# Kernel tuning notes

Hardware: AMD Instinct MI355X
Metric: run time of the kernel (lower is better)

Reference implementation:

```python
import jax, jax.numpy as jnp
import numpy as np

NUM_HEADS = 16


def _qdq(x):
    """Symmetric int8 fake-quant along the last axis (per-token for
    activations, per-output-channel for [out,in] weights). Equivalent math to
    int8 GEMM with dynamic scales: (x_q @ w_q.T) * sx * sw == qdq(x) @ qdq(w).T."""
    s = jnp.maximum(jnp.max(jnp.abs(x), axis=-1, keepdims=True) / 127.0, 1e-8)
    return jnp.clip(jnp.round(x / s), -127.0, 127.0) * s


def setup_inputs() -> dict:
    key = jax.random.key(0)
    ks = jax.random.split(key, 8)
    B, N, M, D = 2, 4096, 512, 2048
    w_std = 0.02
    return {
        "x": jax.random.normal(ks[0], (B, N, D), jnp.float32),
        "cond": jax.random.normal(ks[1], (B, M, D), jnp.float32),
        "wq": jax.random.normal(ks[2], (D, D), jnp.float32) * w_std,
        "bq": jax.random.normal(ks[3], (D,), jnp.float32) * w_std,
        "wkv": jax.random.normal(ks[4], (2 * D, D), jnp.float32) * w_std,
        "bkv": jax.random.normal(ks[5], (2 * D,), jnp.float32) * w_std,
        "wp": jax.random.normal(ks[6], (D, D), jnp.float32) * w_std,
        "bp": jax.random.normal(ks[7], (D,), jnp.float32) * w_std,
    }


def reference(x, cond, wq, bq, wkv, bkv, wp, bp):
    B, N, C = x.shape
    M = cond.shape[1]
    H = NUM_HEADS
    Dh = C // H

    # W8A8 dynamic-scale q projection (per-token act quant, per-channel weight quant)
    q = _qdq(x) @ _qdq(wq).T + bq                      # [B,N,C]
    # fp16-style kv projection
    kv = cond @ wkv.T + bkv                            # [B,M,2C]
    k, v = jnp.split(kv, 2, axis=-1)                   # view(...,2,H,Dh).unbind(2)

    q = q.reshape(B, N, H, Dh)
    k = k.reshape(B, M, H, Dh)
    v = v.reshape(B, M, H, Dh)

    scale = 1.0 / np.sqrt(Dh)
    attn = jax.nn.softmax(jnp.einsum('bnhd,bmhd->bhnm', q, k) * scale, axis=-1)
    o = jnp.einsum('bhnm,bmhd->bnhd', attn, v).reshape(B, N, C)

    # fused quant_sum (per-token requant of attention output) + W8A8 proj
    out = _qdq(o) @ _qdq(wp).T + bp                    # [B,N,C]
    return out
```

## Files before the change

### kernel.cpp

```cpp
#include <hip/hip_runtime.h>
#include <cstdint>
#include <cstddef>


typedef __bf16 bf16_t;
typedef __bf16 bf16x8 __attribute__((ext_vector_type(8)));
typedef float f32x4 __attribute__((ext_vector_type(4)));

__device__ __forceinline__ void gld16(void* lds, const void* g) {
    __builtin_amdgcn_global_load_lds(
        (__attribute__((address_space(1))) uint32_t*)(uintptr_t)g,
        (__attribute__((address_space(3))) uint32_t*)(uint32_t)(uintptr_t)lds,
        16, 0, 0);
}

__device__ __forceinline__ void load8(const float* p, int i, float* v) {
    const float4* p4 = (const float4*)p;
    float4 a = p4[2 * i], b = p4[2 * i + 1];
    v[0] = a.x; v[1] = a.y; v[2] = a.z; v[3] = a.w;
    v[4] = b.x; v[5] = b.y; v[6] = b.z; v[7] = b.w;
}
__device__ __forceinline__ void load8(const bf16_t* p, int i, float* v) {
    bf16x8 t = ((const bf16x8*)p)[i];
#pragma unroll
    for (int j = 0; j < 8; ++j) v[j] = (float)t[j];
}

template <int QUANT, typename T>
__global__ __launch_bounds__(256) void rowpack(const T* __restrict__ in,
                                               bf16_t* __restrict__ out, int K) {
    const int tid = threadIdx.x;
    const size_t row = blockIdx.x;
    const T* rp = in + row * (size_t)K;
    const int n8 = K >> 3;
    float scale = 1.0f;
    if (QUANT) {
        float m = 0.f;
        for (int i = tid; i < n8; i += 256) {
            float v[8];
            load8(rp, i, v);
#pragma unroll
            for (int j = 0; j < 8; ++j) m = fmaxf(m, fabsf(v[j]));
        }
        __shared__ float red[256];
        red[tid] = m;
        __syncthreads();
        for (int s = 128; s > 0; s >>= 1) {
            if (tid < s) red[tid] = fmaxf(red[tid], red[tid + s]);
            __syncthreads();
        }
        scale = fmaxf(red[0] * (1.0f / 127.0f), 1e-8f);
    }
    const int KT = K >> 5;
    const int p = (int)(row >> 7), c = ((int)row >> 4) & 7, lm = (int)row & 15;
    for (int i = tid; i < n8; i += 256) {
        const int col = i << 3;
        const int kt = col >> 5, quad = (col >> 3) & 3;
        float v[8];
        load8(rp, i, v);
        bf16x8 o8;
#pragma unroll
        for (int j = 0; j < 8; ++j) {
            float q = v[j];
            if (QUANT) {
                q = rintf(q / scale);
                q = fminf(127.f, fmaxf(-127.f, q)) * scale;
            }
            o8[j] = (bf16_t)q;
        }
        const size_t dst = ((size_t)(p * KT + kt) * 8 + c) * 512 + (quad * 16 + lm) * 8;
        *(bf16x8*)(out + dst) = o8;
    }
}

template <int MODE>
__global__ __launch_bounds__(256) void gemm_pk(const bf16_t* __restrict__ A,
                                               const bf16_t* __restrict__ B,
                                               const float* __restrict__ bias,
                                               void* __restrict__ C,
                                               int N, int K) {
    __shared__ __align__(16) bf16_t sA[4096];
    __shared__ __align__(16) bf16_t sB[4096];

    const int tid = threadIdx.x;
    const int l = tid & 63, w = tid >> 6;
    const int lm = l & 15, quad = l >> 4;
    const int wm = w & 1, wn = w >> 1;
    const int KT = K >> 5;
    const size_t aBase = (size_t)blockIdx.y * KT * 8 * 512;
    const size_t bBase = (size_t)blockIdx.x * KT * 8 * 512;

    f32x4 acc[4][4] = {};
    for (int kt = 0; kt < KT; ++kt) {
        __syncthreads();
#pragma unroll
        for (int it = 0; it < 2; ++it) {
            const int c = w + it * 4;
            gld16(sA + c * 512, A + aBase + ((size_t)kt * 8 + c) * 512 + l * 8);
            gld16(sB + c * 512, B + bBase + ((size_t)kt * 8 + c) * 512 + l * 8);
        }
        __syncthreads();
        bf16x8 af[4], bfr[4];
#pragma unroll
        for (int i = 0; i < 4; ++i)
            af[i] = *(const bf16x8*)(sA + (wm * 4 + i) * 512 + l * 8);
#pragma unroll
        for (int j = 0; j < 4; ++j)
            bfr[j] = *(const bf16x8*)(sB + (wn * 4 + j) * 512 + l * 8);
#pragma unroll
        for (int i = 0; i < 4; ++i)
#pragma unroll
            for (int j = 0; j < 4; ++j)
                acc[i][j] = __builtin_amdgcn_mfma_f32_16x16x32_bf16(af[i], bfr[j], acc[i][j], 0, 0, 0);
    }
#pragma unroll
    for (int i = 0; i < 4; ++i) {
#pragma unroll
        for (int j = 0; j < 4; ++j) {
            const int col = blockIdx.x * 128 + wn * 64 + j * 16 + lm;
            const float bv = bias[col];
#pragma unroll
            for (int r = 0; r < 4; ++r) {
                const int row = blockIdx.y * 128 + wm * 64 + i * 16 + quad * 4 + r;
                const float v = acc[i][j][r] + bv;
                if (MODE == 1) {
                    ((float*)C)[(size_t)row * N + col] = v;
                } else if (MODE == 0) {
                    const int b = row >> 12, n = row & 4095;
                    const int h = col >> 7, d = col & 127;
                    const int p = n >> 6, mt = (n >> 4) & 3, lmq = n & 15;
                    const int kq = d >> 5, qq = (d >> 3) & 3, jq = d & 7;
                    const size_t idx =
                        (((size_t)(b * 16 + h) * 64 + p) * 16 + kq * 4 + mt) * 512 +
                        (qq * 16 + lmq) * 8 + jq;
                    ((bf16_t*)C)[idx] = (bf16_t)v;
                } else {
                    const int b = row >> 9, m = row & 511;
                    const int half = col >> 11, h = (col >> 7) & 15, d = col & 127;
                    const int t8 = m >> 6;
                    bf16_t* out = (bf16_t*)C;
                    if (half == 0) {
                        const int nt = (m >> 4) & 3, lmk = m & 15;
                        const int kc = d >> 5, qk = (d >> 3) & 3, jk = d & 7;
                        const size_t idx =
                            (((size_t)(b * 16 + h) * 8 + t8) * 16 + kc * 4 + nt) * 512 +
                            (qk * 16 + lmk) * 8 + jk;
                        out[idx] = (bf16_t)v;
                    } else {
                        const int kv2 = (m >> 5) & 1, qv = (m >> 3) & 3, jv = m & 7;
                        const int ntv = d >> 4, lmv = d & 15;
                        const size_t idx = 2097152 +
                            (((size_t)(b * 16 + h) * 8 + t8) * 16 + kv2 * 8 + ntv) * 512 +
                            (qv * 16 + lmv) * 8 + jv;
                        out[idx] = (bf16_t)v;
                    }
                }
            }
        }
    }
}

__global__ __launch_bounds__(256, 2) void attn64(const bf16_t* __restrict__ qpk,
                                                 const bf16_t* __restrict__ kvpk,
                                                 bf16_t* __restrict__ o) {
    constexpr float SCALE = 0.08838834764831845f;
    __shared__ __align__(16) bf16_t sQ[8192];
    __shared__ __align__(16) bf16_t sKV[8192];
    __shared__ __align__(16) bf16_t sP[4096];
    __shared__ float redM[4][64];
    __shared__ float redS[4][64];

    const int tid = threadIdx.x;
    const int l = tid & 63, w = tid >> 6;
    const int lm = l & 15, quad = l >> 4;
    const int b = blockIdx.z, h = blockIdx.y;
    const int p = blockIdx.x;
    const int bh = b * 16 + h;
    const size_t qbase = ((size_t)bh * 64 + p) * 8192;
    const size_t kbase = (size_t)bh * 65536;
    const size_t vbase = 2097152 + (size_t)bh * 65536;

#pragma unroll
    for (int it = 0; it < 4; ++it) {
        const int c = it * 4 + w;
        gld16(sQ + c * 512, qpk + qbase + (size_t)c * 512 + l * 8);
    }

    f32x4 sfr[8][4] = {};
#pragma unroll
    for (int t8 = 0; t8 < 8; ++t8) {
        __syncthreads();
#pragma unroll
        for (int it = 0; it < 4; ++it) {
            const int c = it * 4 + w;
            gld16(sKV + c * 512, kvpk + kbase + ((size_t)t8 * 16 + c) * 512 + l * 8);
        }
        __syncthreads();
#pragma unroll
        for (int kc = 0; kc < 4; ++kc) {
            bf16x8 bb = *(const bf16x8*)(sKV + (kc * 4 + w) * 512 + l * 8);
#pragma unroll
            for (int mt = 0; mt < 4; ++mt) {
                bf16x8 aa = *(const bf16x8*)(sQ + (kc * 4 + mt) * 512 + l * 8);
                sfr[t8][mt] = __builtin_amdgcn_mfma_f32_16x16x32_bf16(aa, bb, sfr[t8][mt], 0, 0, 0);
            }
        }
    }

    float inv[4][4];
    {
        float mymax[4][4];
#pragma unroll
        for (int mt = 0; mt < 4; ++mt)
#pragma unroll
            for (int r = 0; r < 4; ++r) {
                float m = -3.0e38f;
#pragma unroll
                for (int t8 = 0; t8 < 8; ++t8) m = fmaxf(m, sfr[t8][mt][r]);
                m = fmaxf(m, __shfl_xor(m, 1));
                m = fmaxf(m, __shfl_xor(m, 2));
                m = fmaxf(m, __shfl_xor(m, 4));
                m = fmaxf(m, __shfl_xor(m, 8));
                mymax[mt][r] = m;
            }
        if (lm == 0) {
#pragma unroll
            for (int mt = 0; mt < 4; ++mt)
#pragma unroll
                for (int r = 0; r < 4; ++r)
                    redM[w][mt * 16 + quad * 4 + r] = mymax[mt][r];
        }
        __syncthreads();
#pragma unroll
        for (int mt = 0; mt < 4; ++mt)
#pragma unroll
            for (int r = 0; r < 4; ++r) {
                const int row = mt * 16 + quad * 4 + r;
                const float M =
                    fmaxf(fmaxf(redM[0][row], redM[1][row]), fmaxf(redM[2][row], redM[3][row])) *
                    SCALE;
                float s = 0.f;
#pragma unroll
                for (int t8 = 0; t8 < 8; ++t8) {
                    const float pe = __expf(sfr[t8][mt][r] * SCALE - M);
                    sfr[t8][mt][r] = pe;
                    s += pe;
                }
                s += __shfl_xor(s, 1);
                s += __shfl_xor(s, 2);
                s += __shfl_xor(s, 4);
                s += __shfl_xor(s, 8);
                if (lm == 0) redS[w][row] = s;
            }
        __syncthreads();
#pragma unroll
        for (int mt = 0; mt < 4; ++mt)
#pragma unroll
            for (int r = 0; r < 4; ++r) {
                const int row = mt * 16 + quad * 4 + r;
                inv[mt][r] = 1.f / (redS[0][row] + redS[1][row] + redS[2][row] + redS[3][row]);
            }
    }

    f32x4 oc[4][2] = {};
    const int ktd = w >> 1;
    const int quadd = (w & 1) * 2 + (lm >> 3);
    const int jd = lm & 7;
#pragma unroll
    for (int t8 = 0; t8 < 8; ++t8) {
        __syncthreads();
#pragma unroll
        for (int mt = 0; mt < 4; ++mt)
#pragma unroll
            for (int r = 0; r < 4; ++r)
                sP[(mt * 2 + ktd) * 512 + (quadd * 16 + quad * 4 + r) * 8 + jd] =
                    (bf16_t)sfr[t8][mt][r];
#pragma unroll
        for (int it = 0; it < 4; ++it) {
            const int c = it * 4 + w;
            gld16(sKV + c * 512, kvpk + vbase + ((size_t)t8 * 16 + c) * 512 + l * 8);
        }
        __syncthreads();
#pragma unroll
        for (int kv = 0; kv < 2; ++kv) {
            bf16x8 aa[4];
#pragma unroll
            for (int mt = 0; mt < 4; ++mt)
                aa[mt] = *(const bf16x8*)(sP + (mt * 2 + kv) * 512 + l * 8);
#pragma unroll
            for (int ni = 0; ni < 2; ++ni) {
                bf16x8 bb = *(const bf16x8*)(sKV + (kv * 8 + w * 2 + ni) * 512 + l * 8);
#pragma unroll
                for (int mt = 0; mt < 4; ++mt)
                    oc[mt][ni] = __builtin_amdgcn_mfma_f32_16x16x32_bf16(aa[mt], bb, oc[mt][ni], 0, 0, 0);
            }
        }
    }

#pragma unroll
    for (int mt = 0; mt < 4; ++mt)
#pragma unroll
        for (int ni = 0; ni < 2; ++ni)
#pragma unroll
            for (int r = 0; r < 4; ++r) {
                const int row = mt * 16 + quad * 4 + r;
                const int d = w * 32 + ni * 16 + lm;
                o[((size_t)b * 4096 + p * 64 + row) * 2048 + h * 128 + d] =
                    (bf16_t)(oc[mt][ni][r] * inv[mt][r]);
            }
}

extern "C" void kernel_launch(void* const* d_in, const int* in_sizes, int n_in,
                              void* d_out, int out_size, void* d_ws, size_t ws_size,
                              hipStream_t stream) {
    (void)in_sizes; (void)n_in; (void)out_size; (void)ws_size;
    const float* x    = (const float*)d_in[0];
    const float* cond = (const float*)d_in[1];
    const float* wq   = (const float*)d_in[2];
    const float* bq   = (const float*)d_in[3];
    const float* wkv  = (const float*)d_in[4];
    const float* bkv  = (const float*)d_in[5];
    const float* wp   = (const float*)d_in[6];
    const float* bp   = (const float*)d_in[7];

    const size_t MB = 1ull << 20;
    uint8_t* ws = (uint8_t*)d_ws;
    bf16_t* qxpk   = (bf16_t*)(ws + 0);
    bf16_t* qpk    = (bf16_t*)(ws + 32 * MB);
    bf16_t* wqpk   = (bf16_t*)(ws + 64 * MB);
    bf16_t* wkvpk  = (bf16_t*)(ws + 72 * MB);
    bf16_t* wppk   = (bf16_t*)(ws + 88 * MB);
    bf16_t* condpk = (bf16_t*)(ws + 96 * MB);
    bf16_t* kvpk   = (bf16_t*)(ws + 100 * MB);
    bf16_t* o_nat  = qxpk;
    bf16_t* opk    = qpk;

    dim3 blk(256);
    rowpack<1, float><<<8192, blk, 0, stream>>>(x, qxpk, 2048);
    rowpack<1, float><<<2048, blk, 0, stream>>>(wq, wqpk, 2048);
    rowpack<1, float><<<2048, blk, 0, stream>>>(wp, wppk, 2048);
    rowpack<0, float><<<1024, blk, 0, stream>>>(cond, condpk, 2048);
    rowpack<0, float><<<4096, blk, 0, stream>>>(wkv, wkvpk, 2048);
    gemm_pk<0><<<dim3(16, 64), blk, 0, stream>>>(qxpk, wqpk, bq, qpk, 2048, 2048);
    gemm_pk<2><<<dim3(32, 8), blk, 0, stream>>>(condpk, wkvpk, bkv, kvpk, 4096, 2048);
    attn64<<<dim3(64, 16, 2), blk, 0, stream>>>(qpk, kvpk, o_nat);
    rowpack<1, bf16_t><<<8192, blk, 0, stream>>>(o_nat, opk, 2048);
    gemm_pk<1><<<dim3(16, 64), blk, 0, stream>>>(opk, wppk, bp, (float*)d_out, 2048, 2048);
}
```

Baseline: 599.4 us.

## Double K-step per barrier in GEMMs and attention, split KV GEMM rows

The GEMM main loop now loads a 64-wide K slice (two 32-wide sub-steps) between barrier pairs, which halves the number of synchronisations. A new gemm_kv kernel uses 64-row tiles so the KV projection launches 512 blocks instead of 256, filling more CUs. The attention kernel loads 128 K/V rows per barrier and reuses the Q buffer for P, which doubles the KV staging buffer and keeps total LDS about the same. In exchange, each block uses more shared memory in the GEMMs, and gemm_kv keeps the A tile only half as large.

```diff
diff --git a/kernel.cpp b/kernel.cpp
--- a/kernel.cpp
+++ b/kernel.cpp
@@ -74,13 +74,47 @@
 }
 
 template <int MODE>
+__device__ __forceinline__ void epi_store(void* C, int N, int row, int col, float v) {
+    if (MODE == 1) {
+        ((float*)C)[(size_t)row * N + col] = v;
+    } else if (MODE == 0) {
+        const int b = row >> 12, n = row & 4095;
+        const int h = col >> 7, d = col & 127;
+        const int p = n >> 6, mt = (n >> 4) & 3, lmq = n & 15;
+        const int kq = d >> 5, qq = (d >> 3) & 3, jq = d & 7;
+        const size_t idx = (((size_t)(b * 16 + h) * 64 + p) * 16 + kq * 4 + mt) * 512 +
+                           (qq * 16 + lmq) * 8 + jq;
+        ((bf16_t*)C)[idx] = (bf16_t)v;
+    } else {
+        const int b = row >> 9, m = row & 511;
+        const int half = col >> 11, h = (col >> 7) & 15, d = col & 127;
+        const int t8 = m >> 6;
+        bf16_t* out = (bf16_t*)C;
+        if (half == 0) {
+            const int nt = (m >> 4) & 3, lmk = m & 15;
+            const int kc = d >> 5, qk = (d >> 3) & 3, jk = d & 7;
+            const size_t idx = (((size_t)(b * 16 + h) * 8 + t8) * 16 + kc * 4 + nt) * 512 +
+                               (qk * 16 + lmk) * 8 + jk;
+            out[idx] = (bf16_t)v;
+        } else {
+            const int kv2 = (m >> 5) & 1, qv = (m >> 3) & 3, jv = m & 7;
+            const int ntv = d >> 4, lmv = d & 15;
+            const size_t idx = 2097152 +
+                (((size_t)(b * 16 + h) * 8 + t8) * 16 + kv2 * 8 + ntv) * 512 +
+                (qv * 16 + lmv) * 8 + jv;
+            out[idx] = (bf16_t)v;
+        }
+    }
+}
+
+template <int MODE>
 __global__ __launch_bounds__(256) void gemm_pk(const bf16_t* __restrict__ A,
                                                const bf16_t* __restrict__ B,
                                                const float* __restrict__ bias,
                                                void* __restrict__ C,
                                                int N, int K) {
-    __shared__ __align__(16) bf16_t sA[4096];
-    __shared__ __align__(16) bf16_t sB[4096];
+    __shared__ __align__(16) bf16_t sA[8192];
+    __shared__ __align__(16) bf16_t sB[8192];
 
     const int tid = threadIdx.x;
     const int l = tid & 63, w = tid >> 6;
@@ -91,27 +125,32 @@
     const size_t bBase = (size_t)blockIdx.x * KT * 8 * 512;
 
     f32x4 acc[4][4] = {};
-    for (int kt = 0; kt < KT; ++kt) {
-        __syncthreads();
-#pragma unroll
-        for (int it = 0; it < 2; ++it) {
-            const int c = w + it * 4;
-            gld16(sA + c * 512, A + aBase + ((size_t)kt * 8 + c) * 512 + l * 8);
-            gld16(sB + c * 512, B + bBase + ((size_t)kt * 8 + c) * 512 + l * 8);
-        }
-        __syncthreads();
-        bf16x8 af[4], bfr[4];
-#pragma unroll
-        for (int i = 0; i < 4; ++i)
-            af[i] = *(const bf16x8*)(sA + (wm * 4 + i) * 512 + l * 8);
-#pragma unroll
-        for (int j = 0; j < 4; ++j)
-            bfr[j] = *(const bf16x8*)(sB + (wn * 4 + j) * 512 + l * 8);
-#pragma unroll
-        for (int i = 0; i < 4; ++i)
+    const int NIT = K >> 6;
+    for (int kt = 0; kt < NIT; ++kt) {
+        __syncthreads();
+#pragma unroll
+        for (int it = 0; it < 4; ++it) {
+            const int c = it * 4 + w;
+            gld16(sA + c * 512, A + aBase + ((size_t)kt * 16 + c) * 512 + l * 8);
+            gld16(sB + c * 512, B + bBase + ((size_t)kt * 16 + c) * 512 + l * 8);
+        }
+        __syncthreads();
+#pragma unroll
+        for (int h = 0; h < 2; ++h) {
+            bf16x8 af[4], bfr[4];
+#pragma unroll
+            for (int i = 0; i < 4; ++i)
+                af[i] = *(const bf16x8*)(sA + (h * 8 + wm * 4 + i) * 512 + l * 8);
 #pragma unroll
             for (int j = 0; j < 4; ++j)
-                acc[i][j] = __builtin_amdgcn_mfma_f32_16x16x32_bf16(af[i], bfr[j], acc[i][j], 0, 0, 0);
+                bfr[j] = *(const bf16x8*)(sB + (h * 8 + wn * 4 + j) * 512 + l * 8);
+#pragma unroll
+            for (int i = 0; i < 4; ++i)
+#pragma unroll
+                for (int j = 0; j < 4; ++j)
+                    acc[i][j] =
+                        __builtin_amdgcn_mfma_f32_16x16x32_bf16(af[i], bfr[j], acc[i][j], 0, 0, 0);
+        }
     }
 #pragma unroll
     for (int i = 0; i < 4; ++i) {
@@ -122,39 +161,73 @@
 #pragma unroll
             for (int r = 0; r < 4; ++r) {
                 const int row = blockIdx.y * 128 + wm * 64 + i * 16 + quad * 4 + r;
-                const float v = acc[i][j][r] + bv;
-                if (MODE == 1) {
-                    ((float*)C)[(size_t)row * N + col] = v;
-                } else if (MODE == 0) {
-                    const int b = row >> 12, n = row & 4095;
-                    const int h = col >> 7, d = col & 127;
-                    const int p = n >> 6, mt = (n >> 4) & 3, lmq = n & 15;
-                    const int kq = d >> 5, qq = (d >> 3) & 3, jq = d & 7;
-                    const size_t idx =
-                        (((size_t)(b * 16 + h) * 64 + p) * 16 + kq * 4 + mt) * 512 +
-                        (qq * 16 + lmq) * 8 + jq;
-                    ((bf16_t*)C)[idx] = (bf16_t)v;
-                } else {
-                    const int b = row >> 9, m = row & 511;
-                    const int half = col >> 11, h = (col >> 7) & 15, d = col & 127;
-                    const int t8 = m >> 6;
-                    bf16_t* out = (bf16_t*)C;
-                    if (half == 0) {
-                        const int nt = (m >> 4) & 3, lmk = m & 15;
-                        const int kc = d >> 5, qk = (d >> 3) & 3, jk = d & 7;
-                        const size_t idx =
-                            (((size_t)(b * 16 + h) * 8 + t8) * 16 + kc * 4 + nt) * 512 +
-                            (qk * 16 + lmk) * 8 + jk;
-                        out[idx] = (bf16_t)v;
-                    } else {
-                        const int kv2 = (m >> 5) & 1, qv = (m >> 3) & 3, jv = m & 7;
-                        const int ntv = d >> 4, lmv = d & 15;
-                        const size_t idx = 2097152 +
-                            (((size_t)(b * 16 + h) * 8 + t8) * 16 + kv2 * 8 + ntv) * 512 +
-                            (qv * 16 + lmv) * 8 + jv;
-                        out[idx] = (bf16_t)v;
-                    }
-                }
+                epi_store<MODE>(C, N, row, col, acc[i][j][r] + bv);
+            }
+        }
+    }
+}
+
+__global__ __launch_bounds__(256) void gemm_kv(const bf16_t* __restrict__ A,
+                                               const bf16_t* __restrict__ B,
+                                               const float* __restrict__ bias,
+                                               bf16_t* __restrict__ C,
+                                               int N, int K) {
+    __shared__ __align__(16) bf16_t sA[4096];
+    __shared__ __align__(16) bf16_t sB[8192];
+
+    const int tid = threadIdx.x;
+    const int l = tid & 63, w = tid >> 6;
+    const int lm = l & 15, quad = l >> 4;
+    const int wm = w & 1, wn = w >> 1;
+    const int KT = K >> 5;
+    const int p = blockIdx.y >> 1, hh = blockIdx.y & 1;
+    const size_t aPan = (size_t)p * KT * 8 * 512;
+    const size_t bBase = (size_t)blockIdx.x * KT * 8 * 512;
+
+    f32x4 acc[2][4] = {};
+    const int NIT = K >> 6;
+    for (int kt = 0; kt < NIT; ++kt) {
+        __syncthreads();
+#pragma unroll
+        for (int it = 0; it < 2; ++it) {
+            const int lc = it * 4 + w;
+            const int s = lc >> 2, cc = lc & 3;
+            gld16(sA + lc * 512,
+                  A + aPan + ((size_t)(kt * 2 + s) * 8 + hh * 4 + cc) * 512 + l * 8);
+        }
+#pragma unroll
+        for (int it = 0; it < 4; ++it) {
+            const int lc = it * 4 + w;
+            gld16(sB + lc * 512, B + bBase + ((size_t)kt * 16 + lc) * 512 + l * 8);
+        }
+        __syncthreads();
+#pragma unroll
+        for (int s = 0; s < 2; ++s) {
+            bf16x8 af[2], bfr[4];
+#pragma unroll
+            for (int i = 0; i < 2; ++i)
+                af[i] = *(const bf16x8*)(sA + (s * 4 + wm * 2 + i) * 512 + l * 8);
+#pragma unroll
+            for (int j = 0; j < 4; ++j)
+                bfr[j] = *(const bf16x8*)(sB + (s * 8 + wn * 4 + j) * 512 + l * 8);
+#pragma unroll
+            for (int i = 0; i < 2; ++i)
+#pragma unroll
+                for (int j = 0; j < 4; ++j)
+                    acc[i][j] =
+                        __builtin_amdgcn_mfma_f32_16x16x32_bf16(af[i], bfr[j], acc[i][j], 0, 0, 0);
+        }
+    }
+#pragma unroll
+    for (int i = 0; i < 2; ++i) {
+#pragma unroll
+        for (int j = 0; j < 4; ++j) {
+            const int col = blockIdx.x * 128 + wn * 64 + j * 16 + lm;
+            const float bv = bias[col];
+#pragma unroll
+            for (int r = 0; r < 4; ++r) {
+                const int row = blockIdx.y * 64 + wm * 32 + i * 16 + quad * 4 + r;
+                epi_store<2>(C, N, row, col, acc[i][j][r] + bv);
             }
         }
     }
@@ -164,9 +237,8 @@
                                                  const bf16_t* __restrict__ kvpk,
                                                  bf16_t* __restrict__ o) {
     constexpr float SCALE = 0.08838834764831845f;
-    __shared__ __align__(16) bf16_t sQ[8192];
-    __shared__ __align__(16) bf16_t sKV[8192];
-    __shared__ __align__(16) bf16_t sP[4096];
+    __shared__ __align__(16) bf16_t sQP[8192];
+    __shared__ __align__(16) bf16_t sKV[16384];
     __shared__ float redM[4][64];
     __shared__ float redS[4][64];
 
@@ -183,26 +255,30 @@
 #pragma unroll
     for (int it = 0; it < 4; ++it) {
         const int c = it * 4 + w;
-        gld16(sQ + c * 512, qpk + qbase + (size_t)c * 512 + l * 8);
+        gld16(sQP + c * 512, qpk + qbase + (size_t)c * 512 + l * 8);
     }
 
     f32x4 sfr[8][4] = {};
 #pragma unroll
-    for (int t8 = 0; t8 < 8; ++t8) {
-        __syncthreads();
-#pragma unroll
-        for (int it = 0; it < 4; ++it) {
+    for (int g = 0; g < 4; ++g) {
+        __syncthreads();
+#pragma unroll
+        for (int it = 0; it < 8; ++it) {
             const int c = it * 4 + w;
-            gld16(sKV + c * 512, kvpk + kbase + ((size_t)t8 * 16 + c) * 512 + l * 8);
+            gld16(sKV + c * 512, kvpk + kbase + ((size_t)g * 32 + c) * 512 + l * 8);
         }
         __syncthreads();
 #pragma unroll
         for (int kc = 0; kc < 4; ++kc) {
-            bf16x8 bb = *(const bf16x8*)(sKV + (kc * 4 + w) * 512 + l * 8);
-#pragma unroll
-            for (int mt = 0; mt < 4; ++mt) {
-                bf16x8 aa = *(const bf16x8*)(sQ + (kc * 4 + mt) * 512 + l * 8);
-                sfr[t8][mt] = __builtin_amdgcn_mfma_f32_16x16x32_bf16(aa, bb, sfr[t8][mt], 0, 0, 0);
+#pragma unroll
+            for (int kk = 0; kk < 2; ++kk) {
+                bf16x8 bb = *(const bf16x8*)(sKV + (kk * 16 + kc * 4 + w) * 512 + l * 8);
+#pragma unroll
+                for (int mt = 0; mt < 4; ++mt) {
+                    bf16x8 aa = *(const bf16x8*)(sQP + (kc * 4 + mt) * 512 + l * 8);
+                    sfr[g * 2 + kk][mt] =
+                        __builtin_amdgcn_mfma_f32_16x16x32_bf16(aa, bb, sfr[g * 2 + kk][mt], 0, 0, 0);
+                }
             }
         }
     }
@@ -267,32 +343,37 @@
     const int quadd = (w & 1) * 2 + (lm >> 3);
     const int jd = lm & 7;
 #pragma unroll
-    for (int t8 = 0; t8 < 8; ++t8) {
-        __syncthreads();
-#pragma unroll
-        for (int mt = 0; mt < 4; ++mt)
-#pragma unroll
-            for (int r = 0; r < 4; ++r)
-                sP[(mt * 2 + ktd) * 512 + (quadd * 16 + quad * 4 + r) * 8 + jd] =
-                    (bf16_t)sfr[t8][mt][r];
-#pragma unroll
-        for (int it = 0; it < 4; ++it) {
+    for (int g = 0; g < 4; ++g) {
+        __syncthreads();
+#pragma unroll
+        for (int kk = 0; kk < 2; ++kk)
+#pragma unroll
+            for (int mt = 0; mt < 4; ++mt)
+#pragma unroll
+                for (int r = 0; r < 4; ++r)
+                    sQP[(mt * 4 + kk * 2 + ktd) * 512 + (quadd * 16 + quad * 4 + r) * 8 + jd] =
+                        (bf16_t)sfr[g * 2 + kk][mt][r];
+#pragma unroll
+        for (int it = 0; it < 8; ++it) {
             const int c = it * 4 + w;
-            gld16(sKV + c * 512, kvpk + vbase + ((size_t)t8 * 16 + c) * 512 + l * 8);
-        }
-        __syncthreads();
-#pragma unroll
-        for (int kv = 0; kv < 2; ++kv) {
+            gld16(sKV + c * 512, kvpk + vbase + ((size_t)g * 32 + c) * 512 + l * 8);
+        }
+        __syncthreads();
+#pragma unroll
+        for (int kvf = 0; kvf < 4; ++kvf) {
+            const int kk = kvf >> 1, kv2 = kvf & 1;
             bf16x8 aa[4];
 #pragma unroll
             for (int mt = 0; mt < 4; ++mt)
-                aa[mt] = *(const bf16x8*)(sP + (mt * 2 + kv) * 512 + l * 8);
+                aa[mt] = *(const bf16x8*)(sQP + (mt * 4 + kvf) * 512 + l * 8);
 #pragma unroll
             for (int ni = 0; ni < 2; ++ni) {
-                bf16x8 bb = *(const bf16x8*)(sKV + (kv * 8 + w * 2 + ni) * 512 + l * 8);
+                bf16x8 bb =
+                    *(const bf16x8*)(sKV + (kk * 16 + kv2 * 8 + w * 2 + ni) * 512 + l * 8);
 #pragma unroll
                 for (int mt = 0; mt < 4; ++mt)
-                    oc[mt][ni] = __builtin_amdgcn_mfma_f32_16x16x32_bf16(aa[mt], bb, oc[mt][ni], 0, 0, 0);
+                    oc[mt][ni] =
+                        __builtin_amdgcn_mfma_f32_16x16x32_bf16(aa[mt], bb, oc[mt][ni], 0, 0, 0);
             }
         }
     }
@@ -342,7 +423,7 @@
     rowpack<0, float><<<1024, blk, 0, stream>>>(cond, condpk, 2048);
     rowpack<0, float><<<4096, blk, 0, stream>>>(wkv, wkvpk, 2048);
     gemm_pk<0><<<dim3(16, 64), blk, 0, stream>>>(qxpk, wqpk, bq, qpk, 2048, 2048);
-    gemm_pk<2><<<dim3(32, 8), blk, 0, stream>>>(condpk, wkvpk, bkv, kvpk, 4096, 2048);
+    gemm_kv<<<dim3(32, 16), blk, 0, stream>>>(condpk, wkvpk, bkv, kvpk, 4096, 2048);
     attn64<<<dim3(64, 16, 2), blk, 0, stream>>>(qpk, kvpk, o_nat);
     rowpack<1, bf16_t><<<8192, blk, 0, stream>>>(o_nat, opk, 2048);
     gemm_pk<1><<<dim3(16, 64), blk, 0, stream>>>(opk, wppk, bp, (float*)d_out, 2048, 2048);
```

Result: faster. 534.5 us (-10.8%).
